# Kernel tuning notes

Hardware: AMD Instinct MI355X
Metric: run time of the kernel (lower is better)

Reference implementation:

```python
import jax, jax.numpy as jnp
import numpy as np

NTOKENS = 50257
NHID = 1024
TPC = int(np.ceil(np.sqrt(NTOKENS)))          # 225 tokens per class
NCLASSES = int(np.ceil(NTOKENS / TPC))        # 224 classes
BATCH = 2048
INITRANGE = 0.1


def setup_inputs() -> dict:
    key = jax.random.key(0)
    k1, k2, k3, k4 = jax.random.split(key, 4)
    inputs = jax.random.normal(k1, (BATCH, NHID), dtype=jnp.float32)
    labels = jax.random.randint(k2, (BATCH,), 0, NTOKENS, dtype=jnp.int32)
    W_top = jax.random.uniform(k3, (NHID, NCLASSES), dtype=jnp.float32,
                               minval=-INITRANGE, maxval=INITRANGE)
    b_top = jnp.zeros((NCLASSES,), dtype=jnp.float32)
    W_bottom = jax.random.uniform(k4, (NCLASSES, NHID, TPC), dtype=jnp.float32,
                                  minval=-INITRANGE, maxval=INITRANGE)
    b_bottom = jnp.zeros((NCLASSES, TPC), dtype=jnp.float32)
    return {"inputs": inputs, "labels": labels, "W_top": W_top, "b_top": b_top,
            "W_bottom": W_bottom, "b_bottom": b_bottom}


def reference(inputs, labels, W_top, b_top, W_bottom, b_bottom):
    # Two-level hierarchical softmax: P(word) = P(class | h) * P(word | class, h)
    batch = inputs.shape[0]
    cls = labels // TPC          # [B] class index at top level
    word = labels % TPC          # [B] word index within class

    # Top level: [B, nclasses]
    top_probs = jax.nn.softmax(inputs @ W_top + b_top, axis=1)
    p_cls = top_probs[jnp.arange(batch), cls]            # [B]

    # Bottom level: gather per-example class weights then batched matvec
    Wb = W_bottom[cls]                                    # [B, nhid, tpc]
    bb = b_bottom[cls]                                    # [B, tpc]
    bottom_logits = jnp.einsum('bd,bdk->bk', inputs, Wb) + bb
    bottom_probs = jax.nn.softmax(bottom_logits, axis=1)
    p_word = bottom_probs[jnp.arange(batch), word]        # [B]

    return p_cls * p_word
```

## Files before the change

kernel.cpp:

```cpp
#include <hip/hip_runtime.h>
#include <math.h>

#define TPC 225
#define NCLS 224
#define NHID 1024
#define BATCH 2048
#define CAP 256
#define LSTRIDE 256

#define NCHUNK 8
#define CHUNK_D 128
#define NDQ 32

#define TCH 16
#define TCH_D 64
#define TROWS 32
#define TPAD 228

__global__ __launch_bounds__(256) void hs_bucket(const int* __restrict__ labels,
                                                 int* __restrict__ bucket,
                                                 int* __restrict__ cnt) {
    __shared__ int scnt[NCLS];
    const int t = threadIdx.x;
    for (int i = t; i < NCLS; i += 256) scnt[i] = 0;
    __syncthreads();
    for (int b = t; b < BATCH; b += 256) {
        int lab = labels[b];
        int c = lab / TPC;
        int pos = atomicAdd(&scnt[c], 1);
        bucket[c * CAP + pos] = b;
    }
    __syncthreads();
    for (int i = t; i < NCLS; i += 256) cnt[i] = scnt[i];
}

__global__ __launch_bounds__(512, 2) void hs_tlogits(const float* __restrict__ x,
                                                     const float* __restrict__ W,
                                                     float* __restrict__ twsP) {
    __shared__ float lw[TCH_D * TPAD];
    const int rb = blockIdx.x >> 4;
    const int q = blockIdx.x & 15;
    const int t = threadIdx.x;
    const int lane = t & 63;
    const int wv = t >> 6;

    for (int r = wv; r < TCH_D; r += 8) {
        if (lane < 56) {
            float4 v = *(const float4*)(W + (size_t)(q * TCH_D + r) * NCLS + 4 * lane);
            *(float4*)(&lw[r * TPAD + 4 * lane]) = v;
        }
    }
    __syncthreads();

    int rows[4];
#pragma unroll
    for (int rl = 0; rl < 4; rl++) rows[rl] = rb * TROWS + wv * 4 + rl;
    const float* xp[4];
#pragma unroll
    for (int rl = 0; rl < 4; rl++)
        xp[rl] = x + (size_t)rows[rl] * NHID + q * TCH_D;
    int kcl[4];
#pragma unroll
    for (int j = 0; j < 4; j++) {
        int k = lane + 64 * j;
        kcl[j] = (k < NCLS) ? k : (NCLS - 1);
    }

    float acc[4][4] = {};
    for (int dq = 0; dq < TCH_D / 4; ++dq) {
        float w[4][4];
#pragma unroll
        for (int di = 0; di < 4; di++)
#pragma unroll
            for (int j = 0; j < 4; j++)
                w[di][j] = lw[(dq * 4 + di) * TPAD + kcl[j]];
        float4 xq[4];
#pragma unroll
        for (int rl = 0; rl < 4; rl++)
            xq[rl] = *(const float4*)(xp[rl] + dq * 4);
#pragma unroll
        for (int rl = 0; rl < 4; rl++)
#pragma unroll
            for (int di = 0; di < 4; di++) {
                float xv = ((const float*)&xq[rl])[di];
#pragma unroll
                for (int j = 0; j < 4; j++)
                    acc[rl][j] = fmaf(xv, w[di][j], acc[rl][j]);
            }
    }

    float* tp = twsP + (size_t)q * BATCH * LSTRIDE;
#pragma unroll
    for (int rl = 0; rl < 4; rl++)
#pragma unroll
        for (int j = 0; j < 4; j++) {
            int k = lane + 64 * j;
            if (k < NCLS) tp[(size_t)rows[rl] * LSTRIDE + k] = acc[rl][j];
        }
}

template <int RW>
__device__ __forceinline__ void bchunk(const float* __restrict__ xb,
                                       const float* __restrict__ wq,
                                       const int* __restrict__ bucket_c,
                                       const int base, const int n,
                                       const int lane, const int wr,
                                       float* __restrict__ bp) {
    int rows[RW], rval[RW];
#pragma unroll
    for (int rl = 0; rl < RW; rl++) {
        int idx = base + wr * RW + rl;
        rows[rl] = bucket_c[idx < n ? idx : 0];
        rval[rl] = (idx < n);
    }
    const float* xp[RW];
#pragma unroll
    for (int rl = 0; rl < RW; rl++) xp[rl] = xb + (size_t)rows[rl] * NHID;
    const int kb = (4 * lane <= TPC - 4) ? 4 * lane : (TPC - 4);
    const float* pw = wq + kb;

    float acc[RW][4] = {};
    for (int dq = 0; dq < NDQ; ++dq) {
        float4 wv4[4];
#pragma unroll
        for (int di = 0; di < 4; di++)
            wv4[di] = *(const float4*)(pw + di * TPC);
        pw += 4 * TPC;
        float4 xq[RW];
#pragma unroll
        for (int rl = 0; rl < RW; rl++)
            xq[rl] = *(const float4*)(xp[rl] + dq * 4);
#pragma unroll
        for (int rl = 0; rl < RW; rl++)
#pragma unroll
            for (int di = 0; di < 4; di++) {
                const float xv = ((const float*)&xq[rl])[di];
                acc[rl][0] = fmaf(xv, wv4[di].x, acc[rl][0]);
                acc[rl][1] = fmaf(xv, wv4[di].y, acc[rl][1]);
                acc[rl][2] = fmaf(xv, wv4[di].z, acc[rl][2]);
                acc[rl][3] = fmaf(xv, wv4[di].w, acc[rl][3]);
            }
    }
#pragma unroll
    for (int rl = 0; rl < RW; rl++) {
        if (rval[rl]) {
            *(float4*)(bp + (size_t)rows[rl] * LSTRIDE + kb) =
                make_float4(acc[rl][0], acc[rl][1], acc[rl][2], acc[rl][3]);
        }
    }
}

__global__ __launch_bounds__(256, 4) void hs_blogits(const float* __restrict__ x,
                                                     const float* __restrict__ Wb,
                                                     const int* __restrict__ bucket,
                                                     const int* __restrict__ cnt,
                                                     float* __restrict__ bws) {
    const int c = blockIdx.x >> 3;
    const int q = blockIdx.x & 7;
    const int n = cnt[c];
    if (n == 0) return;
    const int lane = threadIdx.x & 63;
    const int wr = threadIdx.x >> 6;
    const float* wq = Wb + (size_t)c * (NHID * TPC) + (size_t)q * CHUNK_D * TPC;
    const float* xb = x + q * CHUNK_D;
    const int* bucket_c = bucket + c * CAP;
    float* bp = bws + (size_t)q * BATCH * LSTRIDE;

    for (int base = 0; base < n; base += 16) {
        int m = n - base;
        if (m > 16) m = 16;
        const int RW = (m + 3) >> 2;
        switch (RW) {
            case 1: bchunk<1>(xb, wq, bucket_c, base, n, lane, wr, bp); break;
            case 2: bchunk<2>(xb, wq, bucket_c, base, n, lane, wr, bp); break;
            case 3: bchunk<3>(xb, wq, bucket_c, base, n, lane, wr, bp); break;
            default: bchunk<4>(xb, wq, bucket_c, base, n, lane, wr, bp); break;
        }
    }
}

__global__ __launch_bounds__(256) void hs_finish(const float* __restrict__ tws,
                                                 const float* __restrict__ bws,
                                                 const int* __restrict__ labels,
                                                 const float* __restrict__ b_top,
                                                 const float* __restrict__ b_bot,
                                                 float* __restrict__ out) {
    const int lane = threadIdx.x & 63;
    const int wave = threadIdx.x >> 6;
    const int row = blockIdx.x * 4 + wave;
    const int label = labels[row];
    const int c = label / TPC;
    const int word = label - c * TPC;

    float p[2];
#pragma unroll
    for (int lvl = 0; lvl < 2; lvl++) {
        const int NS = lvl ? TPC : NCLS;
        const int NP = lvl ? NCHUNK : TCH;
        const int pick = lvl ? word : c;
        const float* lws = lvl ? bws : tws;
        const float* bias = lvl ? (b_bot + c * TPC) : b_top;
        float lg[4];
#pragma unroll
        for (int j = 0; j < 4; j++) {
            int k = lane + 64 * j;
            if (k < NS) {
                float v = 0.f;
                for (int pq = 0; pq < NP; pq++)
                    v += lws[((size_t)pq * BATCH + row) * LSTRIDE + k];
                lg[j] = v + bias[k];
            } else {
                lg[j] = -INFINITY;
            }
        }
        float m = fmaxf(fmaxf(lg[0], lg[1]), fmaxf(lg[2], lg[3]));
#pragma unroll
        for (int off = 32; off > 0; off >>= 1) m = fmaxf(m, __shfl_xor(m, off, 64));
        float s = 0.f, pp = 0.f;
#pragma unroll
        for (int j = 0; j < 4; j++) {
            int k = lane + 64 * j;
            float e = (k < NS) ? __expf(lg[j] - m) : 0.f;
            s += e;
            if (k == pick) pp = e;
        }
#pragma unroll
        for (int off = 32; off > 0; off >>= 1) {
            s += __shfl_xor(s, off, 64);
            pp += __shfl_xor(pp, off, 64);
        }
        p[lvl] = pp / s;
    }
    if (lane == 0) out[row] = p[0] * p[1];
}

extern "C" void kernel_launch(void* const* d_in, const int* in_sizes, int n_in,
                              void* d_out, int out_size, void* d_ws, size_t ws_size,
                              hipStream_t stream) {
    const float* inputs   = (const float*)d_in[0];
    const int*   labels   = (const int*)d_in[1];
    const float* W_top    = (const float*)d_in[2];
    const float* b_top    = (const float*)d_in[3];
    const float* W_bottom = (const float*)d_in[4];
    const float* b_bottom = (const float*)d_in[5];
    float* out = (float*)d_out;

    int* bucket = (int*)d_ws;
    int* cnt    = bucket + NCLS * CAP;
    float* tws  = (float*)(cnt + NCLS);
    float* bws  = tws + (size_t)TCH * BATCH * LSTRIDE;

    hs_bucket<<<1, 256, 0, stream>>>(labels, bucket, cnt);
    hs_tlogits<<<64 * TCH, 512, 0, stream>>>(inputs, W_top, tws);
    hs_blogits<<<NCLS * NCHUNK, 256, 0, stream>>>(inputs, W_bottom, bucket, cnt, bws);
    hs_finish<<<BATCH / 4, 256, 0, stream>>>(tws, bws, labels, b_top, b_bottom, out);
}
```

Baseline: 494.7 us.

## Stage bottom-level class weights in LDS and split hidden dim into 16 chunks

```diff
diff --git a/kernel.cpp b/kernel.cpp
--- a/kernel.cpp
+++ b/kernel.cpp
@@ -8,14 +8,14 @@
 #define CAP 256
 #define LSTRIDE 256
 
-#define NCHUNK 8
-#define CHUNK_D 128
-#define NDQ 32
-
 #define TCH 16
 #define TCH_D 64
 #define TROWS 32
 #define TPAD 228
+
+#define BCH 16
+#define BCH_D 64
+#define BPAD 228
 
 __global__ __launch_bounds__(256) void hs_bucket(const int* __restrict__ labels,
                                                  int* __restrict__ bucket,
@@ -100,32 +100,41 @@
 }
 
 template <int RW>
-__device__ __forceinline__ void bchunk(const float* __restrict__ xb,
-                                       const float* __restrict__ wq,
-                                       const int* __restrict__ bucket_c,
-                                       const int base, const int n,
-                                       const int lane, const int wr,
-                                       float* __restrict__ bp) {
+__device__ __forceinline__ void bcomp(const float* __restrict__ xb,
+                                      const int* __restrict__ bucket_c,
+                                      const int base, const int n,
+                                      const int lane, const int wv,
+                                      const float* __restrict__ lw,
+                                      float* __restrict__ bp) {
     int rows[RW], rval[RW];
 #pragma unroll
     for (int rl = 0; rl < RW; rl++) {
-        int idx = base + wr * RW + rl;
-        rows[rl] = bucket_c[idx < n ? idx : 0];
+        int idx = base + wv + 8 * rl;
+        rows[rl] = bucket_c[idx < n ? idx : (n - 1)];
         rval[rl] = (idx < n);
     }
     const float* xp[RW];
 #pragma unroll
     for (int rl = 0; rl < RW; rl++) xp[rl] = xb + (size_t)rows[rl] * NHID;
-    const int kb = (4 * lane <= TPC - 4) ? 4 * lane : (TPC - 4);
-    const float* pw = wq + kb;
-
-    float acc[RW][4] = {};
-    for (int dq = 0; dq < NDQ; ++dq) {
-        float4 wv4[4];
+    int kcl[4];
+#pragma unroll
+    for (int j = 0; j < 4; j++) {
+        int k = lane + 64 * j;
+        kcl[j] = (k < TPC) ? k : (TPC - 1);
+    }
+    float acc[RW][4];
+#pragma unroll
+    for (int rl = 0; rl < RW; rl++)
+#pragma unroll
+        for (int j = 0; j < 4; j++) acc[rl][j] = 0.f;
+
+    for (int dq = 0; dq < BCH_D / 4; ++dq) {
+        float w[4][4];
 #pragma unroll
         for (int di = 0; di < 4; di++)
-            wv4[di] = *(const float4*)(pw + di * TPC);
-        pw += 4 * TPC;
+#pragma unroll
+            for (int j = 0; j < 4; j++)
+                w[di][j] = lw[(dq * 4 + di) * BPAD + kcl[j]];
         float4 xq[RW];
 #pragma unroll
         for (int rl = 0; rl < RW; rl++)
@@ -134,47 +143,62 @@
         for (int rl = 0; rl < RW; rl++)
 #pragma unroll
             for (int di = 0; di < 4; di++) {
-                const float xv = ((const float*)&xq[rl])[di];
-                acc[rl][0] = fmaf(xv, wv4[di].x, acc[rl][0]);
-                acc[rl][1] = fmaf(xv, wv4[di].y, acc[rl][1]);
-                acc[rl][2] = fmaf(xv, wv4[di].z, acc[rl][2]);
-                acc[rl][3] = fmaf(xv, wv4[di].w, acc[rl][3]);
+                float xv = ((const float*)&xq[rl])[di];
+#pragma unroll
+                for (int j = 0; j < 4; j++)
+                    acc[rl][j] = fmaf(xv, w[di][j], acc[rl][j]);
             }
     }
 #pragma unroll
     for (int rl = 0; rl < RW; rl++) {
         if (rval[rl]) {
-            *(float4*)(bp + (size_t)rows[rl] * LSTRIDE + kb) =
-                make_float4(acc[rl][0], acc[rl][1], acc[rl][2], acc[rl][3]);
-        }
-    }
-}
-
-__global__ __launch_bounds__(256, 4) void hs_blogits(const float* __restrict__ x,
+#pragma unroll
+            for (int j = 0; j < 4; j++) {
+                int k = lane + 64 * j;
+                if (k < TPC) bp[(size_t)rows[rl] * LSTRIDE + k] = acc[rl][j];
+            }
+        }
+    }
+}
+
+__global__ __launch_bounds__(512, 2) void hs_blogits(const float* __restrict__ x,
                                                      const float* __restrict__ Wb,
                                                      const int* __restrict__ bucket,
                                                      const int* __restrict__ cnt,
                                                      float* __restrict__ bws) {
-    const int c = blockIdx.x >> 3;
-    const int q = blockIdx.x & 7;
+    __shared__ float lw[BCH_D * BPAD];
+    const int c = blockIdx.x >> 4;
+    const int q = blockIdx.x & 15;
     const int n = cnt[c];
     if (n == 0) return;
-    const int lane = threadIdx.x & 63;
-    const int wr = threadIdx.x >> 6;
-    const float* wq = Wb + (size_t)c * (NHID * TPC) + (size_t)q * CHUNK_D * TPC;
-    const float* xb = x + q * CHUNK_D;
+    const int t = threadIdx.x;
+    const int lane = t & 63;
+    const int wv = t >> 6;
+
+    const float* wq = Wb + (size_t)c * (NHID * TPC) + (size_t)q * BCH_D * TPC;
+    for (int r = wv; r < BCH_D; r += 8) {
+        if (lane < 56) {
+            float4 v = *(const float4*)(wq + (size_t)r * TPC + 4 * lane);
+            *(float4*)(&lw[r * BPAD + 4 * lane]) = v;
+        } else if (lane == 56) {
+            lw[r * BPAD + 224] = wq[(size_t)r * TPC + 224];
+        }
+    }
+    __syncthreads();
+
+    const float* xb = x + q * BCH_D;
     const int* bucket_c = bucket + c * CAP;
     float* bp = bws + (size_t)q * BATCH * LSTRIDE;
 
-    for (int base = 0; base < n; base += 16) {
+    for (int base = 0; base < n; base += 32) {
         int m = n - base;
-        if (m > 16) m = 16;
-        const int RW = (m + 3) >> 2;
+        if (m > 32) m = 32;
+        const int RW = (m + 7) >> 3;
         switch (RW) {
-            case 1: bchunk<1>(xb, wq, bucket_c, base, n, lane, wr, bp); break;
-            case 2: bchunk<2>(xb, wq, bucket_c, base, n, lane, wr, bp); break;
-            case 3: bchunk<3>(xb, wq, bucket_c, base, n, lane, wr, bp); break;
-            default: bchunk<4>(xb, wq, bucket_c, base, n, lane, wr, bp); break;
+            case 1: bcomp<1>(xb, bucket_c, base, n, lane, wv, lw, bp); break;
+            case 2: bcomp<2>(xb, bucket_c, base, n, lane, wv, lw, bp); break;
+            case 3: bcomp<3>(xb, bucket_c, base, n, lane, wv, lw, bp); break;
+            default: bcomp<4>(xb, bucket_c, base, n, lane, wv, lw, bp); break;
         }
     }
 }
@@ -196,7 +220,6 @@
 #pragma unroll
     for (int lvl = 0; lvl < 2; lvl++) {
         const int NS = lvl ? TPC : NCLS;
-        const int NP = lvl ? NCHUNK : TCH;
         const int pick = lvl ? word : c;
         const float* lws = lvl ? bws : tws;
         const float* bias = lvl ? (b_bot + c * TPC) : b_top;
@@ -206,7 +229,7 @@
             int k = lane + 64 * j;
             if (k < NS) {
                 float v = 0.f;
-                for (int pq = 0; pq < NP; pq++)
+                for (int pq = 0; pq < 16; pq++)
                     v += lws[((size_t)pq * BATCH + row) * LSTRIDE + k];
                 lg[j] = v + bias[k];
             } else {
@@ -252,6 +275,6 @@
 
     hs_bucket<<<1, 256, 0, stream>>>(labels, bucket, cnt);
     hs_tlogits<<<64 * TCH, 512, 0, stream>>>(inputs, W_top, tws);
-    hs_blogits<<<NCLS * NCHUNK, 256, 0, stream>>>(inputs, W_bottom, bucket, cnt, bws);
+    hs_blogits<<<NCLS * BCH, 512, 0, stream>>>(inputs, W_bottom, bucket, cnt, bws);
     hs_finish<<<BATCH / 4, 256, 0, stream>>>(tws, bws, labels, b_top, b_bottom, out);
 }
```

Result: faster. 458.6 us (-7.3%).
